# Performance work log

Measured on AMD Instinct MI355X. Metric: run time of the kernel, lower is better.

Reference implementation:

```python
import jax, jax.numpy as jnp
import numpy as np

B, N, D = 2, 2048, 1024
H = 16
HD = D // H  # 64
N_CTX = 256


def setup_inputs() -> dict:
    key = jax.random.key(0)
    ks = jax.random.split(key, 10)
    x = jax.random.normal(ks[0], (B, N, D), dtype=jnp.float32)
    ctx_ppr = jax.random.uniform(ks[1], (N_CTX,), dtype=jnp.float32, minval=1e-4, maxval=1.0)
    ctx_trust = jax.random.uniform(ks[2], (N_CTX,), dtype=jnp.float32)
    attn_mask = jax.random.randint(ks[3], (N, N), 0, 2).astype(jnp.bool_)
    # parameters (nn.Linear convention: y = x @ W.T + b)
    s_in = 1.0 / np.sqrt(D)
    W_in = jax.random.uniform(ks[4], (3 * D, D), dtype=jnp.float32, minval=-s_in, maxval=s_in)
    b_in = jax.random.uniform(ks[5], (3 * D,), dtype=jnp.float32, minval=-s_in, maxval=s_in)
    W_out = jax.random.uniform(ks[6], (D, D), dtype=jnp.float32, minval=-s_in, maxval=s_in)
    b_out = jax.random.uniform(ks[7], (D,), dtype=jnp.float32, minval=-s_in, maxval=s_in)
    log_ppr_alpha = jnp.ones((1,), jnp.float32) * 0.1
    trust_scale = jnp.ones((1,), jnp.float32) * 0.1
    return {"x": x, "ctx_ppr": ctx_ppr, "ctx_trust": ctx_trust, "n_ctx": N_CTX,
            "attn_mask": attn_mask, "W_in": W_in, "b_in": b_in,
            "W_out": W_out, "b_out": b_out,
            "log_ppr_alpha": log_ppr_alpha, "trust_scale": trust_scale}


def reference(x, ctx_ppr, ctx_trust, n_ctx, attn_mask, W_in, b_in, W_out, b_out,
              log_ppr_alpha, trust_scale):
    Bx, Nx, Dx = x.shape
    scale = HD ** -0.5
    qkv = x @ W_in.T + b_in  # [B,N,3D]
    q, k, v = jnp.split(qkv, 3, axis=-1)
    q = q.reshape(Bx, Nx, H, HD).transpose(0, 2, 1, 3)  # [B,H,N,d]
    k = k.reshape(Bx, Nx, H, HD).transpose(0, 2, 1, 3)
    v = v.reshape(Bx, Nx, H, HD).transpose(0, 2, 1, 3)
    if n_ctx > 0:
        gate = jax.nn.sigmoid(trust_scale[0] * ctx_trust)  # [n_ctx]
        gate_full = jnp.concatenate([gate, jnp.ones(Nx - n_ctx, x.dtype)])
        v = v * gate_full[None, None, :, None]
    logits = jnp.einsum('bhqd,bhkd->bhqk', q, k) * scale
    if n_ctx > 0:
        bias = log_ppr_alpha[0] * jnp.log(jnp.clip(ctx_ppr, 1e-8, None))
        col_bias = jnp.concatenate([bias, jnp.zeros(Nx - n_ctx, x.dtype)])
        logits = logits + col_bias[None, None, None, :]
    logits = jnp.where(attn_mask[None, None, :, :], -jnp.inf, logits)
    weights = jax.nn.softmax(logits, axis=-1)
    out = jnp.einsum('bhqk,bhkd->bhqd', weights, v)
    out = out.transpose(0, 2, 1, 3).reshape(Bx, Nx, Dx)
    return out @ W_out.T + b_out
```

## Files before the change

kernel.cpp:

```cpp
#include <hip/hip_runtime.h>
#include <hip/hip_bf16.h>
#include <math.h>

#define B_   2
#define N_   2048
#define D_   1024
#define H_   16
#define TD_  3072
#define LOG2E 1.44269504088896340736f
#define SCALE_Q (0.125f * LOG2E)

typedef short  bf16x8 __attribute__((ext_vector_type(8)));
typedef _Float16 f16x8 __attribute__((ext_vector_type(8)));
typedef _Float16 f16x4 __attribute__((ext_vector_type(4)));
typedef float  f32x4  __attribute__((ext_vector_type(4)));
typedef float  f32x16 __attribute__((ext_vector_type(16)));

#define MFMA16(a, b, c)   __builtin_amdgcn_mfma_f32_16x16x32_bf16(a, b, c, 0, 0, 0)
#define MFMA32B(a, b, c)  __builtin_amdgcn_mfma_f32_32x32x16_bf16(a, b, c, 0, 0, 0)
#define MFMA32H(a, b, c)  __builtin_amdgcn_mfma_f32_32x32x16_f16(a, b, c, 0, 0, 0)

__device__ __forceinline__ ushort f2bf(float f) {
    union { float f; unsigned u; } v; v.f = f;
    unsigned r = (v.u + 0x7fffu + ((v.u >> 16) & 1u)) >> 16;
    return (ushort)r;
}
__device__ __forceinline__ unsigned pkrtz(float a, float b) {
    typedef __fp16 h2 __attribute__((ext_vector_type(2)));
    union { h2 h; unsigned u; } c;
    c.h = __builtin_amdgcn_cvt_pkrtz(a, b);
    return c.u;
}
__device__ __forceinline__ void async16(const void* g, void* l) {
    __builtin_amdgcn_global_load_lds(
        (const __attribute__((address_space(1))) unsigned*)g,
        (__attribute__((address_space(3))) unsigned*)l, 16, 0, 0);
}
__device__ __forceinline__ void plswap(unsigned &a, unsigned &b) {
    auto r = __builtin_amdgcn_permlane32_swap((int)a, (int)b, false, false);
    a = (unsigned)r[0]; b = (unsigned)r[1];
}

__global__ __launch_bounds__(256) void preprocess(
    const float* __restrict__ x, const float* __restrict__ W_in,
    const float* __restrict__ W_out, const float* __restrict__ ctx_ppr,
    const float* __restrict__ log_alpha, const int* __restrict__ n_ctx_p,
    const int* __restrict__ mask,
    ushort* __restrict__ xb, ushort* __restrict__ wib, ushort* __restrict__ wob,
    float* __restrict__ biasrow, unsigned* __restrict__ maskbits)
{
    const int J0 = 1048576, J1 = 786432, J2 = 262144, JM = 131072, JB = 2048;
    int t = blockIdx.x * 256 + threadIdx.x;
    if (t < J0 + J1 + J2) {
        const float* src; ushort* dst; int i = t;
        if (i < J0)           { src = x;      dst = xb;  }
        else if (i < J0 + J1) { i -= J0;      src = W_in;  dst = wib; }
        else                  { i -= J0 + J1; src = W_out; dst = wob; }
        float4 v = ((const float4*)src)[i];
        ushort4 o;
        o.x = f2bf(v.x); o.y = f2bf(v.y); o.z = f2bf(v.z); o.w = f2bf(v.w);
        ((ushort4*)dst)[i] = o;
    } else if (t < J0 + J1 + J2 + JM) {
        int i = t - (J0 + J1 + J2);
        const int4* m = (const int4*)(mask + (size_t)i * 32);
        unsigned bits = 0u;
        #pragma unroll
        for (int j = 0; j < 8; ++j) {
            int4 w = m[j];
            bits |= (w.x != 0 ? 1u : 0u) << (j * 4 + 0);
            bits |= (w.y != 0 ? 1u : 0u) << (j * 4 + 1);
            bits |= (w.z != 0 ? 1u : 0u) << (j * 4 + 2);
            bits |= (w.w != 0 ? 1u : 0u) << (j * 4 + 3);
        }
        maskbits[i] = bits;
    } else if (t < J0 + J1 + J2 + JM + JB) {
        int k = t - (J0 + J1 + J2 + JM);
        int nc = n_ctx_p[0];
        float bv = 0.f;
        if (k < nc) bv = log_alpha[0] * __log2f(fmaxf(ctx_ppr[k], 1e-8f));
        biasrow[k] = bv;
    }
}

template<int BCOL, int MODE>
__global__ __launch_bounds__(256) void gemm_bt(
    const ushort* __restrict__ A, const ushort* __restrict__ Bw,
    const float* __restrict__ bias, float* __restrict__ Cout,
    ushort* __restrict__ qkout, _Float16* __restrict__ vTout,
    int Ncol, int K,
    const float* __restrict__ ctx_trust, const float* __restrict__ trust_scale,
    const int* __restrict__ n_ctx_p)
{
    constexpr int NT = BCOL / 32;
    __shared__ ushort tA[128 * 32];
    __shared__ ushort tB[BCOL * 32];
    const int tid = threadIdx.x;
    const int lane = tid & 63, wv = tid >> 6;
    const int ln = lane & 15, kg = lane >> 4;
    const int rh = wv >> 1, ch = wv & 1;
    const int row0 = blockIdx.y * 128, col0 = blockIdx.x * BCOL;

    int offA[4], offB[NT];
    #pragma unroll
    for (int i = 0; i < 4; ++i) {
        int ra = rh * 64 + i * 16 + ln;
        offA[i] = ra * 32 + ((kg ^ ((ra >> 1) & 3)) << 3);
    }
    #pragma unroll
    for (int i = 0; i < NT; ++i) {
        int rb = ch * (BCOL / 2) + i * 16 + ln;
        offB[i] = rb * 32 + ((kg ^ ((rb >> 1) & 3)) << 3);
    }
    f32x4 acc[4][NT];
    #pragma unroll
    for (int i = 0; i < 4; ++i)
        #pragma unroll
        for (int j = 0; j < NT; ++j) acc[i][j] = (f32x4){0.f, 0.f, 0.f, 0.f};

    for (int kt = 0; kt < K; kt += 32) {
        __syncthreads();
        #pragma unroll
        for (int r2 = 0; r2 < 2; ++r2) {
            int g = r2 * 256 + tid;
            int row = g >> 2;
            int srck = ((g & 3) ^ ((row >> 1) & 3)) << 3;
            async16(A + (size_t)(row0 + row) * K + kt + srck, &tA[g * 8]);
        }
        #pragma unroll
        for (int r2 = 0; r2 < BCOL / 64; ++r2) {
            int g = r2 * 256 + tid;
            int row = g >> 2;
            int srck = ((g & 3) ^ ((row >> 1) & 3)) << 3;
            async16(Bw + (size_t)(col0 + row) * K + kt + srck, &tB[g * 8]);
        }
        __syncthreads();
        bf16x8 af[4], bfr[NT];
        #pragma unroll
        for (int i = 0; i < 4; ++i)  af[i]  = *(const bf16x8*)&tA[offA[i]];
        #pragma unroll
        for (int i = 0; i < NT; ++i) bfr[i] = *(const bf16x8*)&tB[offB[i]];
        #pragma unroll
        for (int mt = 0; mt < 4; ++mt)
            #pragma unroll
            for (int nt = 0; nt < NT; ++nt)
                acc[mt][nt] = MFMA16(af[mt], bfr[nt], acc[mt][nt]);
    }

    const int nctx = n_ctx_p ? n_ctx_p[0] : 0;
    const float ts = trust_scale ? trust_scale[0] : 0.f;
    #pragma unroll
    for (int nt = 0; nt < NT; ++nt) {
        int col = col0 + ch * (BCOL / 2) + nt * 16 + ln;
        float bv = bias[col];
        #pragma unroll
        for (int mt = 0; mt < 4; ++mt) {
            int rbase = row0 + rh * 64 + mt * 16 + kg * 4;
            f32x4 a = acc[mt][nt];
            if (MODE == 0) {
                #pragma unroll
                for (int reg = 0; reg < 4; ++reg)
                    Cout[(size_t)(rbase + reg) * Ncol + col] = a[reg] + bv;
            } else {
                if (col < D_) {
                    #pragma unroll
                    for (int reg = 0; reg < 4; ++reg)
                        qkout[(size_t)(rbase + reg) * 2048 + col] =
                            f2bf((a[reg] + bv) * SCALE_Q);
                } else if (col < 2 * D_) {
                    #pragma unroll
                    for (int reg = 0; reg < 4; ++reg)
                        qkout[(size_t)(rbase + reg) * 2048 + col] = f2bf(a[reg] + bv);
                } else {
                    int vc = col - 2 * D_;
                    int hh = vc >> 6, dim = vc & 63;
                    int bb = rbase >> 11, nbase = rbase & (N_ - 1);
                    ushort4 o;
                    #pragma unroll
                    for (int reg = 0; reg < 4; ++reg) {
                        float v = a[reg] + bv;
                        int n = nbase + reg;
                        if (n < nctx) {
                            float g = 1.f / (1.f + __expf(-ts * ctx_trust[n]));
                            v *= g;
                        }
                        _Float16 hv = (_Float16)v;
                        ((ushort*)&o)[reg] = *(ushort*)&hv;
                    }
                    *(ushort4*)&vTout[((size_t)(bb * 16 + hh) * 64 + dim) * 2048 + nbase] = o;
                }
            }
        }
    }
}

__global__ __launch_bounds__(256, 4) void attn(
    const ushort* __restrict__ qkb,
    const _Float16* __restrict__ vT,
    const unsigned* __restrict__ maskbits,
    const float* __restrict__ biasrow,
    const int* __restrict__ n_ctx_p,
    _Float16* __restrict__ op0,
    _Float16* __restrict__ op1,
    float* __restrict__ lpart)
{
    __shared__ ushort   Kt[3][64 * 64];
    __shared__ _Float16 Vt[2][64 * 64];
    const int tid = threadIdx.x;
    const int lane = tid & 63, wv = tid >> 6;
    const int q31 = lane & 31, hi = lane >> 5;
    const int b = blockIdx.y >> 4, h = blockIdx.y & 15;
    const int q0w = blockIdx.x * 128 + wv * 32;
    const int kh = blockIdx.z;
    const int kbase = kh << 10;
    const int nctx = n_ctx_p[0];

    bf16x8 qf[4];
    {
        const ushort* qrow = qkb + (size_t)(b * N_ + q0w + q31) * 2048 + h * 64;
        #pragma unroll
        for (int ks = 0; ks < 4; ++ks)
            qf[ks] = *(const bf16x8*)(qrow + ks * 16 + hi * 8);
    }
    const size_t kgbase = (size_t)(b * N_ + kbase) * 2048 + 1024 + h * 64;
    const _Float16* vbase = vT + (size_t)((b * 16 + h) * 64) * 2048 + kbase;
    const unsigned* mrow = maskbits + (size_t)(q0w + q31) * 64 + (kbase >> 5);

    int goff[2], ldso[2];
    #pragma unroll
    for (int r2 = 0; r2 < 2; ++r2) {
        int g = r2 * 256 + tid, row = g >> 3, sg = (g & 7) ^ (row & 7);
        goff[r2] = row * 2048 + sg * 8;
        ldso[r2] = g * 8;
    }

    f32x16 O[2];
    O[0] = (f32x16)(0.f); O[1] = (f32x16)(0.f);
    float lrun = 0.f;

    uint2 mcur = *(const uint2*)&mrow[0];
    asm volatile("" ::: "memory");
    {
        const ushort* gp0 = qkb + kgbase;
        #pragma unroll
        for (int r2 = 0; r2 < 2; ++r2) async16(gp0 + goff[r2], &Kt[0][ldso[r2]]);
        const _Float16* vp = vbase;
        #pragma unroll
        for (int r2 = 0; r2 < 2; ++r2) async16(vp + goff[r2], &Vt[0][ldso[r2]]);
        const ushort* gp1 = qkb + kgbase + (size_t)(64 * 2048);
        #pragma unroll
        for (int r2 = 0; r2 < 2; ++r2) async16(gp1 + goff[r2], &Kt[1][ldso[r2]]);
    }

    const int swz = q31 & 7;
    int kb = 0;
    #pragma unroll 1
    for (int ci = 0; ci < 16; ++ci) {
        asm volatile("s_barrier" ::: "memory");
        uint2 mnext = mcur;
        if (ci < 15) {
            mnext = *(const uint2*)&mrow[(ci + 1) * 2];
            asm volatile("" ::: "memory");
            const _Float16* vp = vbase + (ci + 1) * 64;
            #pragma unroll
            for (int r2 = 0; r2 < 2; ++r2)
                async16(vp + goff[r2], &Vt[(ci + 1) & 1][ldso[r2]]);
        }
        if (ci < 14) {
            int nb = kb + 2; if (nb >= 3) nb -= 3;
            const ushort* gp = qkb + kgbase + (size_t)(ci + 2) * (64 * 2048);
            #pragma unroll
            for (int r2 = 0; r2 < 2; ++r2)
                async16(gp + goff[r2], &Kt[nb][ldso[r2]]);
        }
        if (ci < 14)       asm volatile("s_waitcnt vmcnt(7)" ::: "memory");
        else if (ci == 14) asm volatile("s_waitcnt vmcnt(5)" ::: "memory");
        else               asm volatile("s_waitcnt vmcnt(0)" ::: "memory");
        asm volatile("s_barrier" ::: "memory");

        const ushort*   KT = Kt[kb];
        const _Float16* VT = Vt[ci & 1];
        const int c0g = kbase + ci * 64;
        const bool has_bias = (c0g < nctx);
        unsigned msh[2] = { mcur.x >> (hi * 4), mcur.y >> (hi * 4) };
        float lsum = 0.f;

        #pragma unroll
        for (int t = 0; t < 2; ++t) {
            f32x16 S = (f32x16)(0.f);
            const int rbase = (t * 32 + q31) * 64;
            #pragma unroll
            for (int ks = 0; ks < 4; ++ks) {
                bf16x8 kf = *(const bf16x8*)&KT[rbase + (((ks * 2 + hi) ^ swz) << 3)];
                S = MFMA32B(kf, qf[ks], S);
            }
            float p[16];
            #pragma unroll
            for (int g = 0; g < 4; ++g) {
                f32x4 bb;
                if (has_bias)
                    bb = *(const f32x4*)&biasrow[c0g + t * 32 + g * 8 + hi * 4];
                #pragma unroll
                for (int r = 0; r < 4; ++r) {
                    const int reg = g * 4 + r;
                    const int br = r + 8 * g;
                    float s = S[reg] - 4.f;
                    if (has_bias) s += bb[r];
                    s = ((msh[t] >> br) & 1u) ? -1e30f : s;
                    p[reg] = __builtin_exp2f(s);
                }
            }
            float l0 = (p[0] + p[1]) + (p[2] + p[3]);
            float l1 = (p[4] + p[5]) + (p[6] + p[7]);
            float l2 = (p[8] + p[9]) + (p[10] + p[11]);
            float l3 = (p[12] + p[13]) + (p[14] + p[15]);
            lsum += (l0 + l1) + (l2 + l3);
            unsigned pk[8];
            #pragma unroll
            for (int i = 0; i < 8; ++i)
                pk[i] = pkrtz(p[2 * i], p[2 * i + 1]);

            #pragma unroll
            for (int kss = 0; kss < 2; ++kss) {
                const int ks = 2 * t + kss, lo4 = kss * 4;
                unsigned w0 = pk[lo4 + 0], w1 = pk[lo4 + 1];
                unsigned w2 = pk[lo4 + 2], w3 = pk[lo4 + 3];
                plswap(w0, w2);
                plswap(w1, w3);
                union { f16x8 v; unsigned u[4]; } frag;
                frag.u[0] = w0; frag.u[1] = w1;
                frag.u[2] = w2; frag.u[3] = w3;
                #pragma unroll
                for (int t2 = 0; t2 < 2; ++t2) {
                    const int vb = (t2 * 32 + q31) * 64;
                    union { f16x8 v; int4 i4; } vf;
                    vf.i4 = *(const int4*)&VT[vb + (((ks * 2 + hi) ^ swz) << 3)];
                    O[t2] = MFMA32H(vf.v, frag.v, O[t2]);
                }
            }
        }
        lrun += lsum;
        mcur = mnext;
        kb = kb + 1; if (kb >= 3) kb -= 3;
    }

    float l = lrun + __shfl_xor(lrun, 32);
    float inv = 1.f / l;
    _Float16* orow = (kh ? op1 : op0)
                   + (size_t)(b * N_ + q0w + q31) * 1024 + h * 64;
    #pragma unroll
    for (int t = 0; t < 2; ++t)
        #pragma unroll
        for (int g = 0; g < 4; ++g) {
            ushort4 o;
            #pragma unroll
            for (int r = 0; r < 4; ++r) {
                _Float16 hv = (_Float16)(O[t][g * 4 + r] * inv);
                ((ushort*)&o)[r] = *(ushort*)&hv;
            }
            *(ushort4*)&orow[t * 32 + g * 8 + hi * 4] = o;
        }
    if (hi == 0)
        lpart[(kh << 16) + (b * 16 + h) * 2048 + q0w + q31] = l;
}

__global__ __launch_bounds__(256) void combine(
    const _Float16* __restrict__ op0, const _Float16* __restrict__ op1,
    const float* __restrict__ lpart, ushort* __restrict__ attb)
{
    int t = blockIdx.x * 256 + threadIdx.x;
    size_t idx = (size_t)t * 4;
    int col = (int)(idx & 1023);
    int row = (int)(idx >> 10);
    int h = col >> 6;
    int b = row >> 11, q = row & 2047;
    int lidx = (b * 16 + h) * 2048 + q;
    float l0 = lpart[lidx], l1 = lpart[65536 + lidx];
    float inv = 1.f / (l0 + l1);
    float w0 = l0 * inv, w1 = l1 * inv;
    f16x4 a0 = *(const f16x4*)(op0 + idx);
    f16x4 a1 = *(const f16x4*)(op1 + idx);
    ushort4 o;
    #pragma unroll
    for (int r = 0; r < 4; ++r)
        ((ushort*)&o)[r] = f2bf((float)a0[r] * w0 + (float)a1[r] * w1);
    *(ushort4*)(attb + idx) = o;
}

extern "C" void kernel_launch(void* const* d_in, const int* in_sizes, int n_in,
                              void* d_out, int out_size, void* d_ws, size_t ws_size,
                              hipStream_t stream)
{
    const float* x         = (const float*)d_in[0];
    const float* ctx_ppr   = (const float*)d_in[1];
    const float* ctx_trust = (const float*)d_in[2];
    const int*   n_ctx_p   = (const int*)d_in[3];
    const int*   attn_mask = (const int*)d_in[4];
    const float* W_in      = (const float*)d_in[5];
    const float* b_in      = (const float*)d_in[6];
    const float* W_out     = (const float*)d_in[7];
    const float* b_out     = (const float*)d_in[8];
    const float* log_alpha = (const float*)d_in[9];
    const float* trust_sc  = (const float*)d_in[10];
    float* out = (float*)d_out;

    char* ws = (char*)d_ws;
    ushort*    xb       = (ushort*)ws;    ws += (size_t)4096 * 1024 * 2;
    ushort*    wib      = (ushort*)ws;    ws += (size_t)3072 * 1024 * 2;
    ushort*    wob      = (ushort*)ws;    ws += (size_t)1024 * 1024 * 2;
    ushort*    qkb      = (ushort*)ws;    ws += (size_t)4096 * 2048 * 2;
    _Float16*  vT       = (_Float16*)ws;  ws += (size_t)2048 * 2048 * 2;
    ushort*    attbuf   = (ushort*)ws;    ws += (size_t)4096 * 1024 * 2;
    float*     biasrow  = (float*)ws;     ws += 2048 * 4;
    unsigned*  maskbits = (unsigned*)ws;  ws += (size_t)2048 * 64 * 4;

    _Float16* op0   = (_Float16*)xb;
    _Float16* op1   = (_Float16*)attbuf;
    float*    lpart = (float*)wib;

    hipLaunchKernelGGL(preprocess, dim3(8712), dim3(256), 0, stream,
                       x, W_in, W_out, ctx_ppr, log_alpha, n_ctx_p, attn_mask,
                       xb, wib, wob, biasrow, maskbits);

    hipLaunchKernelGGL((gemm_bt<128, 1>), dim3(24, 32), dim3(256), 0, stream,
                       xb, wib, b_in, (float*)nullptr, qkb, vT, TD_, 1024,
                       ctx_trust, trust_sc, n_ctx_p);

    hipLaunchKernelGGL(attn, dim3(16, 32, 2), dim3(256), 0, stream,
                       qkb, vT, maskbits, biasrow, n_ctx_p, op0, op1, lpart);

    hipLaunchKernelGGL(combine, dim3(4096), dim3(256), 0, stream,
                       op0, op1, lpart, attbuf);

    hipLaunchKernelGGL((gemm_bt<64, 0>), dim3(16, 32), dim3(256), 0, stream,
                       attbuf, wob, b_out, out, (ushort*)nullptr, (_Float16*)nullptr,
                       1024, 1024, ctx_trust, trust_sc, n_ctx_p);
}
```

Baseline: 269.6 us.

## Rotate key-chunk order per block, raise MFMA priority, and use branchless mask select

Each attention block now visits its 16 key/value chunks starting at a rotation offset derived from its linear block index. This spreads concurrent blocks across different K/V memory regions instead of all hitting the same chunk at once. MFMA sections are wrapped in s_setprio so matrix work is favoured over other waves' softmax work. The mask select becomes bit arithmetic, exp uses the raw hardware exp2 builtin, and the constant -4 logit offset is dropped. Dropping the offset and using the raw exp2 slightly raises the risk of fp16 overflow or denormal differences in the probabilities.

```diff
diff --git a/kernel.cpp b/kernel.cpp
--- a/kernel.cpp
+++ b/kernel.cpp
@@ -214,6 +214,13 @@
     const int kbase = kh << 10;
     const int nctx = n_ctx_p[0];
 
+    const int lin = blockIdx.x + (blockIdx.y << 4) + (blockIdx.z << 9);
+    const int rot = ((lin >> 8) << 2) & 15;
+
+    union fi { float f; int i; };
+    fi ng; ng.f = -1e30f;
+    const int NEGI = ng.i;
+
     bf16x8 qf[4];
     {
         const ushort* qrow = qkb + (size_t)(b * N_ + q0w + q31) * 2048 + h * 64;
@@ -237,16 +244,17 @@
     O[0] = (f32x16)(0.f); O[1] = (f32x16)(0.f);
     float lrun = 0.f;
 
-    uint2 mcur = *(const uint2*)&mrow[0];
+    const int cp0 = rot, cp1 = (rot + 1) & 15;
+    uint2 mcur = *(const uint2*)&mrow[cp0 * 2];
     asm volatile("" ::: "memory");
     {
-        const ushort* gp0 = qkb + kgbase;
+        const ushort* gp0 = qkb + kgbase + (size_t)cp0 * (64 * 2048);
         #pragma unroll
         for (int r2 = 0; r2 < 2; ++r2) async16(gp0 + goff[r2], &Kt[0][ldso[r2]]);
-        const _Float16* vp = vbase;
+        const _Float16* vp = vbase + cp0 * 64;
         #pragma unroll
         for (int r2 = 0; r2 < 2; ++r2) async16(vp + goff[r2], &Vt[0][ldso[r2]]);
-        const ushort* gp1 = qkb + kgbase + (size_t)(64 * 2048);
+        const ushort* gp1 = qkb + kgbase + (size_t)cp1 * (64 * 2048);
         #pragma unroll
         for (int r2 = 0; r2 < 2; ++r2) async16(gp1 + goff[r2], &Kt[1][ldso[r2]]);
     }
@@ -258,16 +266,18 @@
         asm volatile("s_barrier" ::: "memory");
         uint2 mnext = mcur;
         if (ci < 15) {
-            mnext = *(const uint2*)&mrow[(ci + 1) * 2];
+            const int cpv = (ci + 1 + rot) & 15;
+            mnext = *(const uint2*)&mrow[cpv * 2];
             asm volatile("" ::: "memory");
-            const _Float16* vp = vbase + (ci + 1) * 64;
+            const _Float16* vp = vbase + cpv * 64;
             #pragma unroll
             for (int r2 = 0; r2 < 2; ++r2)
                 async16(vp + goff[r2], &Vt[(ci + 1) & 1][ldso[r2]]);
         }
         if (ci < 14) {
             int nb = kb + 2; if (nb >= 3) nb -= 3;
-            const ushort* gp = qkb + kgbase + (size_t)(ci + 2) * (64 * 2048);
+            const int cpk = (ci + 2 + rot) & 15;
+            const ushort* gp = qkb + kgbase + (size_t)cpk * (64 * 2048);
             #pragma unroll
             for (int r2 = 0; r2 < 2; ++r2)
                 async16(gp + goff[r2], &Kt[nb][ldso[r2]]);
@@ -279,46 +289,49 @@
 
         const ushort*   KT = Kt[kb];
         const _Float16* VT = Vt[ci & 1];
-        const int c0g = kbase + ci * 64;
+        const int cp = (ci + rot) & 15;
+        const int c0g = kbase + cp * 64;
         const bool has_bias = (c0g < nctx);
-        unsigned msh[2] = { mcur.x >> (hi * 4), mcur.y >> (hi * 4) };
         float lsum = 0.f;
 
         #pragma unroll
         for (int t = 0; t < 2; ++t) {
             f32x16 S = (f32x16)(0.f);
             const int rbase = (t * 32 + q31) * 64;
+            __builtin_amdgcn_s_setprio(1);
             #pragma unroll
             for (int ks = 0; ks < 4; ++ks) {
                 bf16x8 kf = *(const bf16x8*)&KT[rbase + (((ks * 2 + hi) ^ swz) << 3)];
                 S = MFMA32B(kf, qf[ks], S);
             }
-            float p[16];
+            __builtin_amdgcn_s_setprio(0);
+
+            const unsigned msh = (t ? mcur.y : mcur.x) >> (hi * 4);
+            unsigned pk[8];
+            float lt = 0.f;
             #pragma unroll
             for (int g = 0; g < 4; ++g) {
                 f32x4 bb;
                 if (has_bias)
                     bb = *(const f32x4*)&biasrow[c0g + t * 32 + g * 8 + hi * 4];
+                float pr[4];
                 #pragma unroll
                 for (int r = 0; r < 4; ++r) {
-                    const int reg = g * 4 + r;
                     const int br = r + 8 * g;
-                    float s = S[reg] - 4.f;
+                    float s = S[g * 4 + r];
                     if (has_bias) s += bb[r];
-                    s = ((msh[t] >> br) & 1u) ? -1e30f : s;
-                    p[reg] = __builtin_exp2f(s);
+                    int mi = ((int)(msh << (31 - br))) >> 31;
+                    fi su; su.f = s;
+                    su.i = (mi & NEGI) | (su.i & ~mi);
+                    pr[r] = __builtin_amdgcn_exp2f(su.f);
                 }
+                lt += (pr[0] + pr[1]) + (pr[2] + pr[3]);
+                pk[g * 2 + 0] = pkrtz(pr[0], pr[1]);
+                pk[g * 2 + 1] = pkrtz(pr[2], pr[3]);
             }
-            float l0 = (p[0] + p[1]) + (p[2] + p[3]);
-            float l1 = (p[4] + p[5]) + (p[6] + p[7]);
-            float l2 = (p[8] + p[9]) + (p[10] + p[11]);
-            float l3 = (p[12] + p[13]) + (p[14] + p[15]);
-            lsum += (l0 + l1) + (l2 + l3);
-            unsigned pk[8];
-            #pragma unroll
-            for (int i = 0; i < 8; ++i)
-                pk[i] = pkrtz(p[2 * i], p[2 * i + 1]);
-
+            lsum += lt;
+
+            __builtin_amdgcn_s_setprio(1);
             #pragma unroll
             for (int kss = 0; kss < 2; ++kss) {
                 const int ks = 2 * t + kss, lo4 = kss * 4;
@@ -337,6 +350,7 @@
                     O[t2] = MFMA32H(vf.v, frag.v, O[t2]);
                 }
             }
+            __builtin_amdgcn_s_setprio(0);
         }
         lrun += lsum;
         mcur = mnext;
```

Measured after the change: 248.0 us. 8.0% less time.
